# Optimization experiments

Hardware: AMD Instinct MI355X
Metric: run time of the kernel (lower is better)

## Reference

```python
import jax, jax.numpy as jnp
import numpy as np

DIM = 128
HEADS = 4
DIM_HEAD = 32
N_EMBD = HEADS * DIM_HEAD  # 128
SCALE = DIM_HEAD ** -0.5


def conv2d(x, w, b):
    # NCHW conv, 3x3, stride 1, SAME padding (= padding=1 in torch)
    out = jax.lax.conv_general_dilated(
        x, w, window_strides=(1, 1), padding='SAME',
        dimension_numbers=('NCHW', 'OIHW', 'NCHW'))
    return out + b[None, :, None, None]


def conv_block(x, w1, b1, w2, b2):
    # Conv -> ReLU -> Conv (the to_q/to_k/to_v pattern)
    return conv2d(jax.nn.relu(conv2d(x, w1, b1)), w2, b2)


def setup_inputs() -> dict:
    key = jax.random.key(0)
    ks = jax.random.split(key, 20)
    B, C, S = 4, DIM, 32
    H, W = 128, 512
    wscale = 0.05

    def cw(k, cout, cin):
        return jax.random.normal(k, (cout, cin, 3, 3), jnp.float32) * wscale

    inp = {
        'x': jax.random.normal(ks[0], (B, C, S, S), jnp.float32),
        'y': jax.random.normal(ks[1], (B, C, H, W), jnp.float32),
        'u': jax.random.randint(ks[2], (B, S, S), 0, W),
        'q_w1': cw(ks[3], N_EMBD, DIM), 'q_b1': jnp.zeros((N_EMBD,), jnp.float32),
        'q_w2': cw(ks[4], N_EMBD, N_EMBD), 'q_b2': jnp.zeros((N_EMBD,), jnp.float32),
        'k_w1': cw(ks[5], N_EMBD, DIM), 'k_b1': jnp.zeros((N_EMBD,), jnp.float32),
        'k_w2': cw(ks[6], N_EMBD, N_EMBD), 'k_b2': jnp.zeros((N_EMBD,), jnp.float32),
        'v_w1': cw(ks[7], N_EMBD, DIM), 'v_b1': jnp.zeros((N_EMBD,), jnp.float32),
        'v_w2': cw(ks[8], N_EMBD, N_EMBD), 'v_b2': jnp.zeros((N_EMBD,), jnp.float32),
        'proj_w': cw(ks[9], DIM, N_EMBD), 'proj_b': jnp.zeros((DIM,), jnp.float32),
    }
    return inp


def reference(x, y, u, q_w1, q_b1, q_w2, q_b2, k_w1, k_b1, k_w2, k_b2,
              v_w1, v_b1, v_w2, v_b2, proj_w, proj_b):
    B, C, S, _ = x.shape
    _, _, H, W = y.shape
    SS = S * S

    # Q from the (B,C,S,S) query grid -> (B, S^2, n_embd)
    q = conv_block(x, q_w1, q_b1, q_w2, q_b2).reshape(B, N_EMBD, SS).transpose(0, 2, 1)

    # K, V from the (B,C,H,W) map
    k = conv_block(y, k_w1, k_b1, k_w2, k_b2)  # (B, E, H, W)
    v = conv_block(y, v_w1, v_b1, v_w2, v_b2)

    # Gather columns of K/V along W per query index u (clamped)
    uc = jnp.clip(u, 0, W - 1).astype(jnp.int32).reshape(B, 1, 1, SS)
    ks = jnp.take_along_axis(k, uc, axis=3).transpose(0, 3, 2, 1)  # (B, SS, H, E)
    vs = jnp.take_along_axis(v, uc, axis=3).transpose(0, 3, 2, 1)  # (B, SS, H, E)

    # Per-query attention over the H axis
    dot = SCALE * jnp.einsum('bqe,bqhe->bqh', q, ks)  # (B, SS, H)
    attn = jax.nn.softmax(dot, axis=-1)
    a = jnp.einsum('bqh,bqhe->bqe', attn, vs)  # (B, SS, E)

    a = a.transpose(0, 2, 1).reshape(B, N_EMBD, S, S)
    z = jax.nn.relu(conv2d(a, proj_w, proj_b))  # (B, DIM, S, S)
    return z
```

## Files before the change

### kernel.cpp

```cpp
#include <hip/hip_runtime.h>
#include <stdint.h>

typedef __attribute__((ext_vector_type(16))) float f32x16;
typedef __attribute__((ext_vector_type(8))) short s16x8;

#define WAITVM(n) asm volatile("s_waitcnt vmcnt(" #n ")" ::: "memory")
#define WAITLGKM0 asm volatile("s_waitcnt lgkmcnt(0)" ::: "memory")

__device__ inline short bf16b(float f) {
  uint32_t x = __float_as_uint(f);
  return (short)((x + 0x7fffu + ((x >> 16) & 1u)) >> 16);
}
__device__ inline float bfu(uint16_t u) { return __uint_as_float(((uint32_t)u) << 16); }

__device__ inline void gll16(const void* g, void* l) {
  __builtin_amdgcn_global_load_lds((const __attribute__((address_space(1))) void*)g,
                                   (__attribute__((address_space(3))) void*)l, 16, 0, 0);
}

__global__ __launch_bounds__(256) void packw_k(
    const float* w0, const float* w1, const float* w2, const float* w3,
    const float* w4, const float* w5, const float* w6, s16x8* dst) {
  const float* srcs[7] = {w0, w1, w2, w3, w4, w5, w6};
  const int widx = blockIdx.y;
  const float* src = srcs[widx];
  const int gid = blockIdx.x * 256 + threadIdx.x;
  const int lane = gid & 63, frag = gid >> 6;
  const int nblk = frag & 3, ks = (frag >> 2) & 1, chunk = (frag >> 3) & 3, tap = frag >> 5;
  const int co = nblk * 32 + (lane & 31);
  const int cib = chunk * 32 + ks * 16 + (lane >> 5) * 8;
  s16x8 v;
#pragma unroll
  for (int j = 0; j < 8; ++j)
    v[j] = bf16b(src[((size_t)co * 128 + cib + j) * 9 + tap]);
  dst[(size_t)widx * 18432 + (size_t)frag * 64 + lane] = v;
}

template <int TW>
__global__ __launch_bounds__(256) void nchw2nhwc_k(
    const float* __restrict__ in, uint16_t* __restrict__ out, int H, int W) {
  __shared__ float tile[128][TW + 1];
  const int b = blockIdx.z, h = blockIdx.y, w0 = blockIdx.x * TW;
  for (int idx = threadIdx.x; idx < 128 * TW; idx += 256) {
    int c = idx / TW, w = idx - c * TW;
    tile[c][w] = in[(((size_t)b * 128 + c) * H + h) * W + w0 + w];
  }
  __syncthreads();
  for (int idx = threadIdx.x; idx < TW * 16; idx += 256) {
    int w = idx >> 4, cg = idx & 15;
    s16x8 v;
#pragma unroll
    for (int j = 0; j < 8; ++j) v[j] = bf16b(tile[cg * 8 + j][w]);
    *reinterpret_cast<s16x8*>(out + ((((size_t)b * H + h) * W + w0 + w) << 7) + cg * 8) = v;
  }
}

template <int OMODE, bool RELU, typename Tout>
__global__ __launch_bounds__(256, 3) void convmf7_k(
    const uint16_t* __restrict__ in, const s16x8* __restrict__ wpk,
    const float* __restrict__ bias, Tout* __restrict__ out,
    const uint16_t* __restrict__ zp, int H, int W) {
  constexpr int CP = 34, RP = 6, RPCP = RP * CP;
  constexpr int SLOTS = 4 * RPCP;
  constexpr int SPT = 4;
  __shared__ s16x8 lds[2][SPT * 256];
  const int b = blockIdx.z, r0 = blockIdx.y * 4, c0 = blockIdx.x * 32;
  const int tid = threadIdx.x, lane = tid & 63, wn = tid >> 6;
  const int wbase = tid & 192;

  const uint16_t* gsrc[SPT];
#pragma unroll
  for (int i = 0; i < SPT; ++i) {
    const int s = tid + i * 256;
    const int kq = s / RPCP;
    const int rem = s - kq * RPCP;
    const int r = rem / CP, c = rem - r * CP;
    const int gr = r0 + r - 1, gc = c0 + c - 1;
    const bool ok = (s < SLOTS) && gr >= 0 && gr < H && gc >= 0 && gc < W;
    gsrc[i] = ok ? (in + (((size_t)b * H + gr) * W + gc) * 128 + kq * 8) : zp;
  }

  const s16x8* __restrict__ wbl = wpk + wn * 64 + lane;
  s16x8 wf[9];
#pragma unroll
  for (int t = 0; t < 9; ++t) wf[t] = wbl[t * 2048];

#pragma unroll
  for (int i = 0; i < SPT; ++i) gll16(gsrc[i], &lds[0][wbase + i * 256]);

  f32x16 acc[4];
#pragma unroll
  for (int i = 0; i < 4; ++i)
#pragma unroll
    for (int r = 0; r < 16; ++r) acc[i][r] = 0.f;

  const int abase = (lane >> 5) * RPCP + (lane & 31);
  WAITVM(0);
  __builtin_amdgcn_s_barrier();
  __builtin_amdgcn_sched_barrier(0);

#pragma unroll
  for (int chunk = 0; chunk < 4; ++chunk) {
    const int cb = chunk & 1;
    const s16x8* __restrict__ Lb = &lds[cb][abase];
#pragma unroll
    for (int p = 0; p < 6; ++p) {
      const int ks = p / 3, kx = p - ks * 3;
      s16x8 ar[6];
#pragma unroll
      for (int r = 0; r < 6; ++r) ar[r] = Lb[ks * 2 * RPCP + r * CP + kx];
      if (chunk < 3 && p < SPT)
        gll16(gsrc[p] + (chunk + 1) * 32, &lds[cb ^ 1][wbase + p * 256]);
      __builtin_amdgcn_sched_barrier(0);
      __builtin_amdgcn_s_barrier();
      WAITLGKM0;
      __builtin_amdgcn_sched_barrier(0);
      __builtin_amdgcn_s_setprio(1);
#pragma unroll
      for (int ky = 0; ky < 3; ++ky) {
#pragma unroll
        for (int mf = 0; mf < 4; ++mf)
          acc[mf] = __builtin_amdgcn_mfma_f32_32x32x16_bf16(ar[mf + ky], wf[ky * 3 + kx],
                                                            acc[mf], 0, 0, 0);
      }
      __builtin_amdgcn_s_setprio(0);
      if (!(chunk == 3 && ks == 1)) {
        const int nc = (ks == 0) ? chunk : chunk + 1;
        const int nks = (ks == 0) ? 1 : 0;
#pragma unroll
        for (int ky = 0; ky < 3; ++ky) {
          const int tap = ky * 3 + kx;
          wf[tap] = wbl[((tap * 4 + nc) * 2 + nks) * 256];
        }
      }
      __builtin_amdgcn_sched_barrier(0);
      if (p == 5 && chunk < 3) WAITVM(9);
      __builtin_amdgcn_s_barrier();
    }
  }

  const int co = wn * 32 + (lane & 31);
  const float bv = bias[co];
#pragma unroll
  for (int mf = 0; mf < 4; ++mf) {
    const int gr = r0 + mf;
#pragma unroll
    for (int reg = 0; reg < 16; ++reg) {
      const int gc = c0 + (reg & 3) + 8 * (reg >> 2) + 4 * (lane >> 5);
      float v = acc[mf][reg] + bv;
      if (RELU) v = fmaxf(v, 0.f);
      size_t idx;
      if (OMODE == 0)      idx = (((size_t)b * H + gr) * W + gc) * 128 + co;
      else if (OMODE == 1) idx = (((size_t)b * W + gc) * H + gr) * 128 + co;
      else                 idx = (((size_t)b * 128 + co) * H + gr) * W + gc;
      if constexpr (sizeof(Tout) == 2) ((uint16_t*)out)[idx] = (uint16_t)bf16b(v);
      else out[idx] = v;
    }
  }
}

__global__ __launch_bounds__(128) void attn_dot_k(
    const float* __restrict__ qg, const uint16_t* __restrict__ Kg,
    const int* __restrict__ u, float* __restrict__ pout) {
  const int bs = blockIdx.x;
  const int b = bs >> 10;
  const int tid = threadIdx.x;
  __shared__ float sq[128], sd[128];
  sq[tid] = qg[(size_t)bs * 128 + tid];
  int w = u[bs]; w = w < 0 ? 0 : (w > 511 ? 511 : w);
  __syncthreads();
  const uint32_t* kp = reinterpret_cast<const uint32_t*>(
      Kg + (((size_t)b * 512 + w) * 128 + tid) * 128);
  float acc = 0.f;
#pragma unroll 8
  for (int i = 0; i < 64; ++i) {
    uint32_t v = kp[i];
    acc = fmaf(sq[2 * i],     __uint_as_float(v << 16), acc);
    acc = fmaf(sq[2 * i + 1], __uint_as_float(v & 0xffff0000u), acc);
  }
  sd[tid] = acc * 0.17677669529663687f;
  __syncthreads();
  float mx = -1e30f;
  for (int i = 0; i < 128; ++i) mx = fmaxf(mx, sd[i]);
  float e = expf(sd[tid] - mx);
  __syncthreads();
  sd[tid] = e;
  __syncthreads();
  float sum = 0.f;
  for (int i = 0; i < 128; ++i) sum += sd[i];
  pout[(size_t)bs * 128 + tid] = e / sum;
}

__global__ __launch_bounds__(128) void attn_pv_k(
    const float* __restrict__ pin, const uint16_t* __restrict__ Vg,
    const int* __restrict__ u, uint16_t* __restrict__ aout) {
  const int bs = blockIdx.x;
  const int b = bs >> 10;
  const int tid = threadIdx.x;
  __shared__ float sp[128];
  sp[tid] = pin[(size_t)bs * 128 + tid];
  int w = u[bs]; w = w < 0 ? 0 : (w > 511 ? 511 : w);
  __syncthreads();
  const uint16_t* vp = Vg + ((size_t)b * 512 + w) * 16384 + tid;
  float acc = 0.f;
#pragma unroll 8
  for (int h = 0; h < 128; ++h)
    acc = fmaf(sp[h], bfu(vp[h * 128]), acc);
  aout[(size_t)bs * 128 + tid] = (uint16_t)bf16b(acc);
}

extern "C" void kernel_launch(void* const* d_in, const int* in_sizes, int n_in,
                              void* d_out, int out_size, void* d_ws, size_t ws_size,
                              hipStream_t stream) {
  const float* x      = (const float*)d_in[0];
  const float* y      = (const float*)d_in[1];
  const int*   u      = (const int*)d_in[2];
  const float* q_w1   = (const float*)d_in[3];
  const float* q_b1   = (const float*)d_in[4];
  const float* q_w2   = (const float*)d_in[5];
  const float* q_b2   = (const float*)d_in[6];
  const float* k_w1   = (const float*)d_in[7];
  const float* k_b1   = (const float*)d_in[8];
  const float* k_w2   = (const float*)d_in[9];
  const float* k_b2   = (const float*)d_in[10];
  const float* v_w1   = (const float*)d_in[11];
  const float* v_b1   = (const float*)d_in[12];
  const float* v_w2   = (const float*)d_in[13];
  const float* v_b2   = (const float*)d_in[14];
  const float* proj_w = (const float*)d_in[15];
  const float* proj_b = (const float*)d_in[16];
  float* out = (float*)d_out;

  char* ws = (char*)d_ws;
  const size_t MB = 1 << 20;
  const size_t BIG = 64 * MB;
  const bool tierB = ws_size >= 203 * MB;
  uint16_t* A  = (uint16_t*)ws;
  uint16_t* Bb = (uint16_t*)(ws + BIG);
  uint16_t* KV = tierB ? (uint16_t*)(ws + 2 * BIG) : A;
  char* sm = ws + (tierB ? 3 : 2) * BIG;
  float*    qg  = (float*)sm;
  float*    pb  = (float*)(sm + 2 * MB);
  uint16_t* xbf = (uint16_t*)(sm + 4 * MB);
  uint16_t* t1  = (uint16_t*)(sm + 5 * MB);
  uint16_t* ab  = (uint16_t*)(sm + 6 * MB);
  s16x8*    wpk = (s16x8*)(sm + 7 * MB);
  uint16_t* zp  = (uint16_t*)(sm + 10 * MB);

  hipMemsetAsync(zp, 0, 1024, stream);
  packw_k<<<dim3(72, 7), 256, 0, stream>>>(q_w1, q_w2, k_w1, k_w2, v_w1, v_w2, proj_w, wpk);
  nchw2nhwc_k<32><<<dim3(1, 32, 4), 256, 0, stream>>>(x, xbf, 32, 32);
  nchw2nhwc_k<64><<<dim3(8, 128, 4), 256, 0, stream>>>(y, A, 128, 512);
  convmf7_k<0, true,  uint16_t><<<dim3(1, 8, 4), 256, 0, stream>>>(xbf, wpk + 0 * 18432, q_b1, t1, zp, 32, 32);
  convmf7_k<0, false, float   ><<<dim3(1, 8, 4), 256, 0, stream>>>(t1,  wpk + 1 * 18432, q_b2, qg, zp, 32, 32);
  convmf7_k<0, true,  uint16_t><<<dim3(16, 32, 4), 256, 0, stream>>>(A,  wpk + 2 * 18432, k_b1, Bb, zp, 128, 512);
  convmf7_k<1, false, uint16_t><<<dim3(16, 32, 4), 256, 0, stream>>>(Bb, wpk + 3 * 18432, k_b2, KV, zp, 128, 512);
  attn_dot_k<<<dim3(4096), 128, 0, stream>>>(qg, KV, u, pb);
  if (!tierB) nchw2nhwc_k<64><<<dim3(8, 128, 4), 256, 0, stream>>>(y, A, 128, 512);
  convmf7_k<0, true,  uint16_t><<<dim3(16, 32, 4), 256, 0, stream>>>(A,  wpk + 4 * 18432, v_b1, Bb, zp, 128, 512);
  convmf7_k<1, false, uint16_t><<<dim3(16, 32, 4), 256, 0, stream>>>(Bb, wpk + 5 * 18432, v_b2, KV, zp, 128, 512);
  attn_pv_k<<<dim3(4096), 128, 0, stream>>>(pb, KV, u, ab);
  convmf7_k<3, true, float><<<dim3(1, 8, 4), 256, 0, stream>>>(ab, wpk + 6 * 18432, proj_b, out, zp, 32, 32);
}
```

Baseline: 434.5 us.

## Deepen conv register pipeline and vectorize attention dot/PV kernels

The conv kernel now keeps weights for both k-subslices of a chunk in registers and processes three kx passes per chunk instead of six. It keeps one block barrier per chunk rather than two per pass and lowers the occupancy hint from 3 to 2 blocks to make room for the extra registers. The attention dot kernel loads K with 16-byte vector reads and replaces the serial LDS max/sum loops with wavefront shuffle reductions. The PV kernel splits the H axis across thread groups with vector loads and reduces partial sums in LDS. Occupancy drops in exchange for fewer synchronisations and wider memory accesses.

```diff
diff --git a/kernel.cpp b/kernel.cpp
--- a/kernel.cpp
+++ b/kernel.cpp
@@ -56,7 +56,7 @@
 }
 
 template <int OMODE, bool RELU, typename Tout>
-__global__ __launch_bounds__(256, 3) void convmf7_k(
+__global__ __launch_bounds__(256, 2) void convmf8_k(
     const uint16_t* __restrict__ in, const s16x8* __restrict__ wpk,
     const float* __restrict__ bias, Tout* __restrict__ out,
     const uint16_t* __restrict__ zp, int H, int W) {
@@ -81,9 +81,11 @@
   }
 
   const s16x8* __restrict__ wbl = wpk + wn * 64 + lane;
-  s16x8 wf[9];
-#pragma unroll
-  for (int t = 0; t < 9; ++t) wf[t] = wbl[t * 2048];
+  s16x8 wf[2][9];
+#pragma unroll
+  for (int ks = 0; ks < 2; ++ks)
+#pragma unroll
+    for (int t = 0; t < 9; ++t) wf[ks][t] = wbl[(t * 8 + ks) * 256];
 
 #pragma unroll
   for (int i = 0; i < SPT; ++i) gll16(gsrc[i], &lds[0][wbase + i * 256]);
@@ -104,38 +106,47 @@
     const int cb = chunk & 1;
     const s16x8* __restrict__ Lb = &lds[cb][abase];
 #pragma unroll
-    for (int p = 0; p < 6; ++p) {
-      const int ks = p / 3, kx = p - ks * 3;
-      s16x8 ar[6];
-#pragma unroll
-      for (int r = 0; r < 6; ++r) ar[r] = Lb[ks * 2 * RPCP + r * CP + kx];
-      if (chunk < 3 && p < SPT)
-        gll16(gsrc[p] + (chunk + 1) * 32, &lds[cb ^ 1][wbase + p * 256]);
-      __builtin_amdgcn_sched_barrier(0);
-      __builtin_amdgcn_s_barrier();
+    for (int p = 0; p < 3; ++p) {
+      const int kx = p;
+      s16x8 ar[2][6];
+#pragma unroll
+      for (int ks = 0; ks < 2; ++ks)
+#pragma unroll
+        for (int r = 0; r < 6; ++r) ar[ks][r] = Lb[ks * 2 * RPCP + r * CP + kx];
+      if (chunk < 3 && p < 2) {
+        gll16(gsrc[2 * p] + (chunk + 1) * 32, &lds[cb ^ 1][wbase + (2 * p) * 256]);
+        gll16(gsrc[2 * p + 1] + (chunk + 1) * 32, &lds[cb ^ 1][wbase + (2 * p + 1) * 256]);
+      }
+      __builtin_amdgcn_sched_barrier(0);
       WAITLGKM0;
       __builtin_amdgcn_sched_barrier(0);
       __builtin_amdgcn_s_setprio(1);
 #pragma unroll
-      for (int ky = 0; ky < 3; ++ky) {
-#pragma unroll
-        for (int mf = 0; mf < 4; ++mf)
-          acc[mf] = __builtin_amdgcn_mfma_f32_32x32x16_bf16(ar[mf + ky], wf[ky * 3 + kx],
-                                                            acc[mf], 0, 0, 0);
+      for (int ks = 0; ks < 2; ++ks) {
+#pragma unroll
+        for (int ky = 0; ky < 3; ++ky) {
+#pragma unroll
+          for (int mf = 0; mf < 4; ++mf)
+            acc[mf] = __builtin_amdgcn_mfma_f32_32x32x16_bf16(ar[ks][mf + ky], wf[ks][ky * 3 + kx],
+                                                              acc[mf], 0, 0, 0);
+        }
       }
       __builtin_amdgcn_s_setprio(0);
-      if (!(chunk == 3 && ks == 1)) {
-        const int nc = (ks == 0) ? chunk : chunk + 1;
-        const int nks = (ks == 0) ? 1 : 0;
-#pragma unroll
-        for (int ky = 0; ky < 3; ++ky) {
-          const int tap = ky * 3 + kx;
-          wf[tap] = wbl[((tap * 4 + nc) * 2 + nks) * 256];
-        }
+      if (chunk < 3) {
+#pragma unroll
+        for (int ks = 0; ks < 2; ++ks)
+#pragma unroll
+          for (int ky = 0; ky < 3; ++ky) {
+            const int tap = ky * 3 + kx;
+            wf[ks][tap] = wbl[((tap * 4 + chunk + 1) * 2 + ks) * 256];
+          }
       }
       __builtin_amdgcn_sched_barrier(0);
-      if (p == 5 && chunk < 3) WAITVM(9);
+    }
+    if (chunk < 3) {
+      WAITVM(12);
       __builtin_amdgcn_s_barrier();
+      __builtin_amdgcn_sched_barrier(0);
     }
   }
 
@@ -165,30 +176,36 @@
   const int bs = blockIdx.x;
   const int b = bs >> 10;
   const int tid = threadIdx.x;
-  __shared__ float sq[128], sd[128];
+  __shared__ float sq[128];
+  __shared__ float wred[2][2];
   sq[tid] = qg[(size_t)bs * 128 + tid];
   int w = u[bs]; w = w < 0 ? 0 : (w > 511 ? 511 : w);
   __syncthreads();
-  const uint32_t* kp = reinterpret_cast<const uint32_t*>(
+  const s16x8* kp = reinterpret_cast<const s16x8*>(
       Kg + (((size_t)b * 512 + w) * 128 + tid) * 128);
   float acc = 0.f;
-#pragma unroll 8
-  for (int i = 0; i < 64; ++i) {
-    uint32_t v = kp[i];
-    acc = fmaf(sq[2 * i],     __uint_as_float(v << 16), acc);
-    acc = fmaf(sq[2 * i + 1], __uint_as_float(v & 0xffff0000u), acc);
-  }
-  sd[tid] = acc * 0.17677669529663687f;
-  __syncthreads();
-  float mx = -1e30f;
-  for (int i = 0; i < 128; ++i) mx = fmaxf(mx, sd[i]);
-  float e = expf(sd[tid] - mx);
-  __syncthreads();
-  sd[tid] = e;
-  __syncthreads();
-  float sum = 0.f;
-  for (int i = 0; i < 128; ++i) sum += sd[i];
-  pout[(size_t)bs * 128 + tid] = e / sum;
+#pragma unroll
+  for (int i = 0; i < 16; ++i) {
+    s16x8 v = kp[i];
+#pragma unroll
+    for (int j = 0; j < 8; ++j)
+      acc = fmaf(sq[i * 8 + j], bfu((uint16_t)v[j]), acc);
+  }
+  const float d = acc * 0.17677669529663687f;
+  float m = d;
+#pragma unroll
+  for (int o = 1; o < 64; o <<= 1) m = fmaxf(m, __shfl_xor(m, o));
+  if ((tid & 63) == 0) wred[0][tid >> 6] = m;
+  __syncthreads();
+  m = fmaxf(wred[0][0], wred[0][1]);
+  const float e = expf(d - m);
+  float s = e;
+#pragma unroll
+  for (int o = 1; o < 64; o <<= 1) s += __shfl_xor(s, o);
+  if ((tid & 63) == 0) wred[1][tid >> 6] = s;
+  __syncthreads();
+  s = wred[1][0] + wred[1][1];
+  pout[(size_t)bs * 128 + tid] = e / s;
 }
 
 __global__ __launch_bounds__(128) void attn_pv_k(
@@ -197,16 +214,32 @@
   const int bs = blockIdx.x;
   const int b = bs >> 10;
   const int tid = threadIdx.x;
+  const int eo = tid & 15, hg = tid >> 4;
   __shared__ float sp[128];
+  __shared__ float red[8][128];
   sp[tid] = pin[(size_t)bs * 128 + tid];
   int w = u[bs]; w = w < 0 ? 0 : (w > 511 ? 511 : w);
   __syncthreads();
-  const uint16_t* vp = Vg + ((size_t)b * 512 + w) * 16384 + tid;
-  float acc = 0.f;
-#pragma unroll 8
-  for (int h = 0; h < 128; ++h)
-    acc = fmaf(sp[h], bfu(vp[h * 128]), acc);
-  aout[(size_t)bs * 128 + tid] = (uint16_t)bf16b(acc);
+  const s16x8* vp = reinterpret_cast<const s16x8*>(
+      Vg + ((size_t)b * 512 + w) * 16384) + eo;
+  float a8[8];
+#pragma unroll
+  for (int j = 0; j < 8; ++j) a8[j] = 0.f;
+#pragma unroll
+  for (int hh = 0; hh < 16; ++hh) {
+    const int h = hg * 16 + hh;
+    s16x8 v = vp[h * 16];
+    const float p = sp[h];
+#pragma unroll
+    for (int j = 0; j < 8; ++j) a8[j] = fmaf(p, bfu((uint16_t)v[j]), a8[j]);
+  }
+#pragma unroll
+  for (int j = 0; j < 8; ++j) red[hg][eo * 8 + j] = a8[j];
+  __syncthreads();
+  float r = 0.f;
+#pragma unroll
+  for (int g = 0; g < 8; ++g) r += red[g][tid];
+  aout[(size_t)bs * 128 + tid] = (uint16_t)bf16b(r);
 }
 
 extern "C" void kernel_launch(void* const* d_in, const int* in_sizes, int n_in,
@@ -251,14 +284,14 @@
   packw_k<<<dim3(72, 7), 256, 0, stream>>>(q_w1, q_w2, k_w1, k_w2, v_w1, v_w2, proj_w, wpk);
   nchw2nhwc_k<32><<<dim3(1, 32, 4), 256, 0, stream>>>(x, xbf, 32, 32);
   nchw2nhwc_k<64><<<dim3(8, 128, 4), 256, 0, stream>>>(y, A, 128, 512);
-  convmf7_k<0, true,  uint16_t><<<dim3(1, 8, 4), 256, 0, stream>>>(xbf, wpk + 0 * 18432, q_b1, t1, zp, 32, 32);
-  convmf7_k<0, false, float   ><<<dim3(1, 8, 4), 256, 0, stream>>>(t1,  wpk + 1 * 18432, q_b2, qg, zp, 32, 32);
-  convmf7_k<0, true,  uint16_t><<<dim3(16, 32, 4), 256, 0, stream>>>(A,  wpk + 2 * 18432, k_b1, Bb, zp, 128, 512);
-  convmf7_k<1, false, uint16_t><<<dim3(16, 32, 4), 256, 0, stream>>>(Bb, wpk + 3 * 18432, k_b2, KV, zp, 128, 512);
+  convmf8_k<0, true,  uint16_t><<<dim3(1, 8, 4), 256, 0, stream>>>(xbf, wpk + 0 * 18432, q_b1, t1, zp, 32, 32);
+  convmf8_k<0, false, float   ><<<dim3(1, 8, 4), 256, 0, stream>>>(t1,  wpk + 1 * 18432, q_b2, qg, zp, 32, 32);
+  convmf8_k<0, true,  uint16_t><<<dim3(16, 32, 4), 256, 0, stream>>>(A,  wpk + 2 * 18432, k_b1, Bb, zp, 128, 512);
+  convmf8_k<1, false, uint16_t><<<dim3(16, 32, 4), 256, 0, stream>>>(Bb, wpk + 3 * 18432, k_b2, KV, zp, 128, 512);
   attn_dot_k<<<dim3(4096), 128, 0, stream>>>(qg, KV, u, pb);
   if (!tierB) nchw2nhwc_k<64><<<dim3(8, 128, 4), 256, 0, stream>>>(y, A, 128, 512);
-  convmf7_k<0, true,  uint16_t><<<dim3(16, 32, 4), 256, 0, stream>>>(A,  wpk + 4 * 18432, v_b1, Bb, zp, 128, 512);
-  convmf7_k<1, false, uint16_t><<<dim3(16, 32, 4), 256, 0, stream>>>(Bb, wpk + 5 * 18432, v_b2, KV, zp, 128, 512);
+  convmf8_k<0, true,  uint16_t><<<dim3(16, 32, 4), 256, 0, stream>>>(A,  wpk + 4 * 18432, v_b1, Bb, zp, 128, 512);
+  convmf8_k<1, false, uint16_t><<<dim3(16, 32, 4), 256, 0, stream>>>(Bb, wpk + 5 * 18432, v_b2, KV, zp, 128, 512);
   attn_pv_k<<<dim3(4096), 128, 0, stream>>>(pb, KV, u, ab);
-  convmf7_k<3, true, float><<<dim3(1, 8, 4), 256, 0, stream>>>(ab, wpk + 6 * 18432, proj_b, out, zp, 32, 32);
-}
+  convmf8_k<3, true, float><<<dim3(1, 8, 4), 256, 0, stream>>>(ab, wpk + 6 * 18432, proj_b, out, zp, 32, 32);
+}
```

Result: slower. 446.7 us (+2.8%).
